# Kernel optimization log

Measured on AMD Instinct MI355X. Metric: run time of the kernel, lower is better.

The kernel has to match this reference:

```python
import jax, jax.numpy as jnp
import numpy as np

N_HEAD, D_MODEL, D_K, D_V = 16, 1024, 64, 64
LN_EPS = 1e-5


def setup_inputs() -> dict:
    key = jax.random.key(0)
    ks = jax.random.split(key, 7)
    B, L = 2, 2048
    q = jax.random.normal(ks[0], (B, L, N_HEAD * D_K), dtype=jnp.float32)
    k = jax.random.normal(ks[1], (B, L, N_HEAD * D_K), dtype=jnp.float32)
    v = jax.random.normal(ks[2], (B, L, N_HEAD * D_V), dtype=jnp.float32)
    # fc: Linear(d_v*n_head -> d_model)
    lim = 1.0 / np.sqrt(N_HEAD * D_V)
    W_fc = jax.random.uniform(ks[3], (N_HEAD * D_V, D_MODEL), minval=-lim, maxval=lim, dtype=jnp.float32)
    b_fc = jax.random.uniform(ks[4], (D_MODEL,), minval=-lim, maxval=lim, dtype=jnp.float32)
    ln_gamma = jnp.ones((D_MODEL,), dtype=jnp.float32)
    ln_beta = jnp.zeros((D_MODEL,), dtype=jnp.float32)
    return {"q": q, "k": k, "v": v, "W_fc": W_fc, "b_fc": b_fc,
            "ln_gamma": ln_gamma, "ln_beta": ln_beta}


def reference(q, k, v, W_fc, b_fc, ln_gamma, ln_beta):
    B, Lq, _ = q.shape
    Lk = k.shape[1]
    residual = q
    # split heads: [B, L, H*D] -> [B, H, L, D]
    qh = q.reshape(B, Lq, N_HEAD, D_K).transpose(0, 2, 1, 3)
    kh = k.reshape(B, Lk, N_HEAD, D_K).transpose(0, 2, 1, 3)
    vh = v.reshape(B, Lk, N_HEAD, D_V).transpose(0, 2, 1, 3)
    temperature = jnp.sqrt(jnp.asarray(D_K, dtype=q.dtype))
    # [B, H, Lq, Lk] attention scores (materialized, as in the original)
    scores = jnp.einsum('bhqd,bhkd->bhqk', qh, kh) / temperature
    attn = jax.nn.softmax(scores, axis=-1)
    # dropout is identity at eval time
    out = jnp.einsum('bhqk,bhkd->bhqd', attn, vh)
    out = out.transpose(0, 2, 1, 3).reshape(B, Lq, N_HEAD * D_V)
    out = out @ W_fc + b_fc
    out = out + residual
    # LayerNorm over d_model
    mu = jnp.mean(out, axis=-1, keepdims=True)
    var = jnp.var(out, axis=-1, keepdims=True)
    out = (out - mu) * jax.lax.rsqrt(var + LN_EPS) * ln_gamma + ln_beta
    return (out, attn)
```

## Files before the change

kernel.cpp:

```cpp
#include <hip/hip_runtime.h>
#include <hip/hip_bf16.h>
#include <math.h>

#define B_      2
#define L_      2048
#define H_      16
#define DMODEL_ 1024
#define LN_EPS  1e-5f

typedef __attribute__((ext_vector_type(8))) __bf16 bf16x8;
typedef __attribute__((ext_vector_type(8))) short  short8;
typedef __attribute__((ext_vector_type(4))) short  short4_t;
typedef __attribute__((ext_vector_type(4))) float  f32x4;

typedef const __attribute__((address_space(1))) void cgvoid_t;
typedef __attribute__((address_space(3))) void svoid_t;

__device__ __forceinline__ void gload16(const void* g, void* l) {
    __builtin_amdgcn_global_load_lds((cgvoid_t*)g, (svoid_t*)l, 16, 0, 0);
}
__device__ __forceinline__ short f2bf(float x) {
    __hip_bfloat16 h = __float2bfloat16(x);
    return __builtin_bit_cast(short, h);
}
__device__ __forceinline__ float bf2f(short s) {
    unsigned u = ((unsigned)(unsigned short)s) << 16;
    return __builtin_bit_cast(float, u);
}
__device__ __forceinline__ f32x4 mfma16(bf16x8 a, bf16x8 b, f32x4 c) {
    return __builtin_amdgcn_mfma_f32_16x16x32_bf16(a, b, c, 0, 0, 0);
}

__global__ __launch_bounds__(256) void prep_qk(const float* __restrict__ src,
                                               short* __restrict__ dst)
{
    const int t = blockIdx.x * 256 + threadIdx.x;
    const int c = t & 7, l = (t >> 3) & 2047, h = (t >> 14) & 15, b = t >> 18;
    const float* s = src + ((size_t)(b * L_ + l)) * DMODEL_ + h * 64 + c * 8;
    float4 f0 = *(const float4*)s;
    float4 f1 = *(const float4*)(s + 4);
    short8 o;
    o[0] = f2bf(f0.x); o[1] = f2bf(f0.y); o[2] = f2bf(f0.z); o[3] = f2bf(f0.w);
    o[4] = f2bf(f1.x); o[5] = f2bf(f1.y); o[6] = f2bf(f1.z); o[7] = f2bf(f1.w);
    short* d = dst + ((size_t)((b * H_ + h) * L_ + l)) * 64 + (c ^ (l & 7)) * 8;
    *(short8*)d = o;
}

__global__ __launch_bounds__(256) void prep_v(const float* __restrict__ src,
                                              short* __restrict__ dst)
{
    const int blk = blockIdx.x;
    const int g = blk & 63, h = (blk >> 6) & 15, b = blk >> 10;
    const int d = threadIdx.x & 63, lc = g * 4 + (threadIdx.x >> 6);
    const int l0 = lc * 8;
    const float* s = src + ((size_t)(b * L_ + l0)) * DMODEL_ + h * 64 + d;
    short8 o;
    #pragma unroll
    for (int j = 0; j < 8; ++j) o[j] = f2bf(s[(size_t)j * DMODEL_]);
    short* dp = dst + ((size_t)((b * H_ + h) * 64 + d)) * L_
              + (l0 & ~63) + (((lc & 7) ^ (d & 7)) * 8);
    *(short8*)dp = o;
}

__global__ __launch_bounds__(256) void prep_w(const float* __restrict__ W,
                                              short* __restrict__ Wh,
                                              short* __restrict__ Wl)
{
    const int t = blockIdx.x * 256 + threadIdx.x;
    const int n = t & 1023, kc = t >> 10;
    short8 oh, ol;
    #pragma unroll
    for (int e = 0; e < 8; ++e) {
        float wv = W[(size_t)(kc * 8 + e) * 1024 + n];
        short hs = f2bf(wv);
        oh[e] = hs;
        ol[e] = f2bf(wv - bf2f(hs));
    }
    const size_t off = (size_t)n * 1024 + (kc >> 3) * 64 + (((kc & 7) ^ (n & 7)) * 8);
    *(short8*)(Wh + off) = oh;
    *(short8*)(Wl + off) = ol;
}

__global__ __launch_bounds__(256) void attn_mfma(
    const short* __restrict__ Qb, const short* __restrict__ Kb,
    const short* __restrict__ Vb, float* __restrict__ attn,
    short* __restrict__ head)
{
    const int bid = blockIdx.x;
    const int g = (bid & 7) * 128 + (bid >> 3);
    const int qt = g & 31, bh = g >> 5;
    const int h = bh & 15, b = bh >> 4;

    const int tid = threadIdx.x;
    const int lane = tid & 63, w = tid >> 6;
    const int kgrp = lane >> 4, l15 = lane & 15;
    const int q0 = qt * 64;

    __shared__ short qe_s[64 * 64];
    __shared__ short k2_s[2 * 64 * 64];
    __shared__ short v2_s[2 * 64 * 64];

    const char* Qg = (const char*)(Qb + ((size_t)bh * L_ + q0) * 64);
    const char* Kg = (const char*)(Kb + (size_t)bh * L_ * 64);
    const char* Vg = (const char*)(Vb + (size_t)bh * 64 * L_);

    gload16(Qg + (w * 64 + lane) * 16, (char*)qe_s + w * 1024 + lane * 16);
    gload16(Qg + 4096 + (w * 64 + lane) * 16,
            (char*)qe_s + 4096 + w * 1024 + lane * 16);
    __syncthreads();

    const int prow = w * 16 + l15;
    bf16x8 bq0 = *(const bf16x8*)((const char*)qe_s + prow * 128 + ((kgrp ^ (prow & 7)) * 16));
    bf16x8 bq1 = *(const bf16x8*)((const char*)qe_s + prow * 128 + (((kgrp + 4) ^ (prow & 7)) * 16));
    __syncthreads();

    auto stageK = [&](int kt, int bu) {
        const char* kg = Kg + (size_t)kt * 8192;
        char* lk = (char*)k2_s + bu * 8192;
        gload16(kg + (w * 64 + lane) * 16, lk + w * 1024 + lane * 16);
        gload16(kg + 4096 + (w * 64 + lane) * 16, lk + 4096 + w * 1024 + lane * 16);
    };
    auto stageV = [&](int kt, int bu) {
        const char* vg = Vg + (size_t)kt * 128;
        char* lv = (char*)v2_s + bu * 8192;
        int cid = w * 64 + lane;
        gload16(vg + (size_t)(cid >> 3) * 4096 + (cid & 7) * 16, lv + w * 1024 + lane * 16);
        cid += 256;
        gload16(vg + (size_t)(cid >> 3) * 4096 + (cid & 7) * 16, lv + 4096 + w * 1024 + lane * 16);
    };

    float rsum = 0.f;
    stageK(0, 0);
    __syncthreads();
    int buf = 0;
    for (int kt = 0; kt < 32; ++kt) {
        if (kt < 31) stageK(kt + 1, buf ^ 1);
        const char* ks = (const char*)k2_s + buf * 8192;
        #pragma unroll
        for (int t = 0; t < 4; ++t) {
            const int brow = t * 16 + l15;
            f32x4 acc = {0.f, 0.f, 0.f, 0.f};
            bf16x8 k0 = *(const bf16x8*)(ks + brow * 128 + ((kgrp ^ (brow & 7)) * 16));
            bf16x8 k1 = *(const bf16x8*)(ks + brow * 128 + (((kgrp + 4) ^ (brow & 7)) * 16));
            acc = mfma16(k0, bq0, acc);
            acc = mfma16(k1, bq1, acc);
            #pragma unroll
            for (int r = 0; r < 4; ++r) rsum += __expf(acc[r] * 0.125f);
        }
        __syncthreads();
        buf ^= 1;
    }
    rsum += __shfl_xor(rsum, 16, 64);
    rsum += __shfl_xor(rsum, 32, 64);
    const float rinv = 1.0f / rsum;

    f32x4 oacc[4];
    #pragma unroll
    for (int t = 0; t < 4; ++t) oacc[t] = (f32x4){0.f, 0.f, 0.f, 0.f};

    float* arow_p = attn + ((size_t)bh * L_ + q0 + prow) * L_;
    char* pbase = (char*)qe_s + prow * 128;
    const int pswz0 = (kgrp ^ (prow & 7)) * 16;
    const int pswz1 = ((kgrp + 4) ^ (prow & 7)) * 16;

    stageK(0, 0);
    stageV(0, 0);
    __syncthreads();
    buf = 0;
    for (int kt = 0; kt < 32; ++kt) {
        if (kt < 31) { stageK(kt + 1, buf ^ 1); stageV(kt + 1, buf ^ 1); }
        const char* ks = (const char*)k2_s + buf * 8192;
        const char* vs = (const char*)v2_s + buf * 8192;
        #pragma unroll
        for (int t = 0; t < 4; ++t) {
            const int brow = t * 16 + l15;
            f32x4 acc = {0.f, 0.f, 0.f, 0.f};
            bf16x8 k0 = *(const bf16x8*)(ks + brow * 128 + ((kgrp ^ (brow & 7)) * 16));
            bf16x8 k1 = *(const bf16x8*)(ks + brow * 128 + (((kgrp + 4) ^ (brow & 7)) * 16));
            acc = mfma16(k0, bq0, acc);
            acc = mfma16(k1, bq1, acc);
            f32x4 ev;
            ev[0] = __expf(acc[0] * 0.125f) * rinv;
            ev[1] = __expf(acc[1] * 0.125f) * rinv;
            ev[2] = __expf(acc[2] * 0.125f) * rinv;
            ev[3] = __expf(acc[3] * 0.125f) * rinv;
            __builtin_nontemporal_store(ev,
                (f32x4*)(arow_p + kt * 64 + t * 16 + kgrp * 4));
            short4_t pk;
            pk[0] = f2bf(ev[0]); pk[1] = f2bf(ev[1]);
            pk[2] = f2bf(ev[2]); pk[3] = f2bf(ev[3]);
            const int pc = (t * 2 + (kgrp >> 1)) ^ (prow & 7);
            *(short4_t*)((char*)qe_s + prow * 128 + pc * 16 + (kgrp & 1) * 8) = pk;
        }
        bf16x8 pa0 = *(const bf16x8*)(pbase + pswz0);
        bf16x8 pa1 = *(const bf16x8*)(pbase + pswz1);
        #pragma unroll
        for (int t = 0; t < 4; ++t) {
            const int brow = t * 16 + l15;
            bf16x8 v0 = *(const bf16x8*)(vs + brow * 128 + ((kgrp ^ (brow & 7)) * 16));
            bf16x8 v1 = *(const bf16x8*)(vs + brow * 128 + (((kgrp + 4) ^ (brow & 7)) * 16));
            oacc[t] = mfma16(pa0, v0, oacc[t]);
            oacc[t] = mfma16(pa1, v1, oacc[t]);
        }
        __syncthreads();
        buf ^= 1;
    }

    #pragma unroll
    for (int t = 0; t < 4; ++t) {
        #pragma unroll
        for (int r = 0; r < 4; ++r) {
            const int rowidx = b * L_ + q0 + w * 16 + kgrp * 4 + r;
            const int dl = t * 16 + l15;
            head[(size_t)rowidx * 1024 + h * 64
                 + (((dl >> 3) ^ (rowidx & 7)) * 8) + (dl & 7)] = f2bf(oacc[t][r]);
        }
    }
}

__global__ __launch_bounds__(256) void fc_mfma(
    const short* __restrict__ Xs, const short* __restrict__ Wh,
    const short* __restrict__ Wl, const float* __restrict__ bias,
    const float* __restrict__ Qres, float* __restrict__ Y)
{
    const int n0 = blockIdx.x * 64, tok0 = blockIdx.y * 64;
    const int tid = threadIdx.x;
    const int lane = tid & 63, w = tid >> 6;
    const int kgrp = lane >> 4, l15 = lane & 15;

    __shared__ short x2_s[2 * 64 * 64];
    __shared__ short wh2_s[2 * 64 * 64];
    __shared__ short wl2_s[2 * 64 * 64];

    auto stageX = [&](int kt, int bu) {
        const char* xg = (const char*)Xs + (size_t)tok0 * 2048 + kt * 128;
        char* lx = (char*)x2_s + bu * 8192;
        int cid = w * 64 + lane;
        gload16(xg + (size_t)(cid >> 3) * 2048 + (cid & 7) * 16, lx + w * 1024 + lane * 16);
        cid += 256;
        gload16(xg + (size_t)(cid >> 3) * 2048 + (cid & 7) * 16, lx + 4096 + w * 1024 + lane * 16);
    };
    auto stageW = [&](int kt, int bu) {
        const char* wgh = (const char*)Wh + (size_t)n0 * 2048 + kt * 128;
        const char* wgl = (const char*)Wl + (size_t)n0 * 2048 + kt * 128;
        char* lh = (char*)wh2_s + bu * 8192;
        char* ll = (char*)wl2_s + bu * 8192;
        int cid = w * 64 + lane;
        const int ldst = w * 1024 + lane * 16;
        size_t go = (size_t)(cid >> 3) * 2048 + (cid & 7) * 16;
        gload16(wgh + go, lh + ldst);
        gload16(wgl + go, ll + ldst);
        cid += 256;
        go = (size_t)(cid >> 3) * 2048 + (cid & 7) * 16;
        gload16(wgh + go, lh + 4096 + ldst);
        gload16(wgl + go, ll + 4096 + ldst);
    };

    f32x4 oacc[4];
    #pragma unroll
    for (int t = 0; t < 4; ++t) oacc[t] = (f32x4){0.f, 0.f, 0.f, 0.f};

    stageX(0, 0);
    stageW(0, 0);
    __syncthreads();
    int buf = 0;
    const int xrow = w * 16 + l15;
    for (int kt = 0; kt < 16; ++kt) {
        if (kt < 15) { stageX(kt + 1, buf ^ 1); stageW(kt + 1, buf ^ 1); }
        const char* xs = (const char*)x2_s + buf * 8192;
        const char* wh = (const char*)wh2_s + buf * 8192;
        const char* wl = (const char*)wl2_s + buf * 8192;
        bf16x8 bx0 = *(const bf16x8*)(xs + xrow * 128 + ((kgrp ^ (xrow & 7)) * 16));
        bf16x8 bx1 = *(const bf16x8*)(xs + xrow * 128 + (((kgrp + 4) ^ (xrow & 7)) * 16));
        #pragma unroll
        for (int nt = 0; nt < 4; ++nt) {
            const int wrow = nt * 16 + l15;
            const int s0 = wrow * 128 + ((kgrp ^ (wrow & 7)) * 16);
            const int s1 = wrow * 128 + (((kgrp + 4) ^ (wrow & 7)) * 16);
            oacc[nt] = mfma16(*(const bf16x8*)(wh + s0), bx0, oacc[nt]);
            oacc[nt] = mfma16(*(const bf16x8*)(wh + s1), bx1, oacc[nt]);
            oacc[nt] = mfma16(*(const bf16x8*)(wl + s0), bx0, oacc[nt]);
            oacc[nt] = mfma16(*(const bf16x8*)(wl + s1), bx1, oacc[nt]);
        }
        __syncthreads();
        buf ^= 1;
    }

    const int tok = tok0 + w * 16 + l15;
    #pragma unroll
    for (int nt = 0; nt < 4; ++nt) {
        const int n = n0 + nt * 16 + kgrp * 4;
        float4 bb = *(const float4*)(bias + n);
        float4 qq = *(const float4*)(Qres + (size_t)tok * DMODEL_ + n);
        float4 yy;
        yy.x = oacc[nt][0] + bb.x + qq.x;
        yy.y = oacc[nt][1] + bb.y + qq.y;
        yy.z = oacc[nt][2] + bb.z + qq.z;
        yy.w = oacc[nt][3] + bb.w + qq.w;
        *(float4*)(Y + (size_t)tok * DMODEL_ + n) = yy;
    }
}

__global__ __launch_bounds__(256) void ln_kernel(
    const float* __restrict__ Y, const float* __restrict__ gamma,
    const float* __restrict__ beta, float* __restrict__ Out)
{
    const int tok = blockIdx.x * 4 + (threadIdx.x >> 6);
    const int lane = threadIdx.x & 63;
    const float4* yp = (const float4*)(Y + (size_t)tok * DMODEL_);
    float4 vv[4];
    float s = 0.f, s2 = 0.f;
    #pragma unroll
    for (int i = 0; i < 4; ++i) {
        vv[i] = yp[i * 64 + lane];
        s  += vv[i].x + vv[i].y + vv[i].z + vv[i].w;
        s2 += vv[i].x * vv[i].x + vv[i].y * vv[i].y
            + vv[i].z * vv[i].z + vv[i].w * vv[i].w;
    }
    #pragma unroll
    for (int m = 1; m < 64; m <<= 1) {
        s  += __shfl_xor(s,  m, 64);
        s2 += __shfl_xor(s2, m, 64);
    }
    const float mu   = s * (1.f / DMODEL_);
    const float var  = s2 * (1.f / DMODEL_) - mu * mu;
    const float rstd = rsqrtf(var + LN_EPS);
    const float4* g4 = (const float4*)gamma;
    const float4* b4 = (const float4*)beta;
    float4* op = (float4*)(Out + (size_t)tok * DMODEL_);
    #pragma unroll
    for (int i = 0; i < 4; ++i) {
        const int idx = i * 64 + lane;
        float4 g = g4[idx], be = b4[idx], o;
        o.x = (vv[i].x - mu) * rstd * g.x + be.x;
        o.y = (vv[i].y - mu) * rstd * g.y + be.y;
        o.z = (vv[i].z - mu) * rstd * g.z + be.z;
        o.w = (vv[i].w - mu) * rstd * g.w + be.w;
        op[idx] = o;
    }
}

extern "C" void kernel_launch(void* const* d_in, const int* in_sizes, int n_in,
                              void* d_out, int out_size, void* d_ws, size_t ws_size,
                              hipStream_t stream)
{
    const float* q     = (const float*)d_in[0];
    const float* k     = (const float*)d_in[1];
    const float* v     = (const float*)d_in[2];
    const float* W_fc  = (const float*)d_in[3];
    const float* b_fc  = (const float*)d_in[4];
    const float* gamma = (const float*)d_in[5];
    const float* beta  = (const float*)d_in[6];

    char* ws = (char*)d_ws;
    short* qb   = (short*)(ws);
    short* kb   = (short*)(ws + 8388608);
    short* vb   = (short*)(ws + 16777216);
    short* head = (short*)(ws + 25165824);
    short* whi  = (short*)(ws + 33554432);
    short* wlo  = (short*)(ws + 35651584);
    float* y    = (float*)(ws + 37748736);

    float* out  = (float*)d_out;
    float* attn = out + (size_t)B_ * L_ * DMODEL_;

    prep_qk<<<2048, 256, 0, stream>>>(q, qb);
    prep_qk<<<2048, 256, 0, stream>>>(k, kb);
    prep_v <<<2048, 256, 0, stream>>>(v, vb);
    prep_w <<<512,  256, 0, stream>>>(W_fc, whi, wlo);

    attn_mfma<<<1024, 256, 0, stream>>>(qb, kb, vb, attn, head);

    fc_mfma<<<dim3(16, 64), 256, 0, stream>>>(head, whi, wlo, b_fc, q, y);

    ln_kernel<<<1024, 256, 0, stream>>>(y, gamma, beta, out);
}
```

Measured before the change: 731.6 us.

## Double query tile per block, transpose V via shared memory, raise MFMA priority

The attention and FC kernels now run 512 threads (8 waves) per block and cover 128 query/token rows each, so every staged K/V or W tile is reused by twice as many rows and global staging traffic drops. prep_v now stages a 64x64 fp32 tile in padded shared memory and writes the transpose from there, replacing the old strided per-element global reads. s_setprio is raised around the MFMA loops so matrix work wins issue over other waves. The larger blocks use more LDS and registers, which may cut occupancy and halve the block count.

```diff
diff --git a/kernel.cpp b/kernel.cpp
--- a/kernel.cpp
+++ b/kernel.cpp
@@ -50,16 +50,37 @@
                                               short* __restrict__ dst)
 {
     const int blk = blockIdx.x;
-    const int g = blk & 63, h = (blk >> 6) & 15, b = blk >> 10;
-    const int d = threadIdx.x & 63, lc = g * 4 + (threadIdx.x >> 6);
-    const int l0 = lc * 8;
-    const float* s = src + ((size_t)(b * L_ + l0)) * DMODEL_ + h * 64 + d;
-    short8 o;
-    #pragma unroll
-    for (int j = 0; j < 8; ++j) o[j] = f2bf(s[(size_t)j * DMODEL_]);
-    short* dp = dst + ((size_t)((b * H_ + h) * 64 + d)) * L_
-              + (l0 & ~63) + (((lc & 7) ^ (d & 7)) * 8);
-    *(short8*)dp = o;
+    const int lt = blk & 31, h = (blk >> 5) & 15, b = blk >> 9;
+    const int l0 = lt * 64;
+    const int t = threadIdx.x;
+
+    __shared__ float tile[64][65];
+
+    {
+        const int row = t >> 2, seg = t & 3;
+        const float4* s = (const float4*)(src
+            + ((size_t)(b * L_ + l0 + row)) * DMODEL_ + h * 64 + seg * 16);
+        #pragma unroll
+        for (int i = 0; i < 4; ++i) {
+            float4 v = s[i];
+            tile[row][seg * 16 + i * 4 + 0] = v.x;
+            tile[row][seg * 16 + i * 4 + 1] = v.y;
+            tile[row][seg * 16 + i * 4 + 2] = v.z;
+            tile[row][seg * 16 + i * 4 + 3] = v.w;
+        }
+    }
+    __syncthreads();
+
+    const int d = t >> 2, p = t & 3;
+    short* drow = dst + ((size_t)((b * H_ + h) * 64 + d)) * L_ + l0;
+    #pragma unroll
+    for (int cc = 0; cc < 2; ++cc) {
+        const int c = p + cc * 4;
+        short8 o;
+        #pragma unroll
+        for (int j = 0; j < 8; ++j) o[j] = f2bf(tile[c * 8 + j][d]);
+        *(short8*)(drow + ((c ^ (d & 7)) * 8)) = o;
+    }
 }
 
 __global__ __launch_bounds__(256) void prep_w(const float* __restrict__ W,
@@ -81,22 +102,22 @@
     *(short8*)(Wl + off) = ol;
 }
 
-__global__ __launch_bounds__(256) void attn_mfma(
+__global__ __launch_bounds__(512) void attn_mfma(
     const short* __restrict__ Qb, const short* __restrict__ Kb,
     const short* __restrict__ Vb, float* __restrict__ attn,
     short* __restrict__ head)
 {
     const int bid = blockIdx.x;
-    const int g = (bid & 7) * 128 + (bid >> 3);
-    const int qt = g & 31, bh = g >> 5;
+    const int g = (bid & 7) * 64 + (bid >> 3);
+    const int qt = g & 15, bh = g >> 4;
     const int h = bh & 15, b = bh >> 4;
 
     const int tid = threadIdx.x;
     const int lane = tid & 63, w = tid >> 6;
     const int kgrp = lane >> 4, l15 = lane & 15;
-    const int q0 = qt * 64;
-
-    __shared__ short qe_s[64 * 64];
+    const int q0 = qt * 128;
+
+    __shared__ short qe_s[128 * 64];
     __shared__ short k2_s[2 * 64 * 64];
     __shared__ short v2_s[2 * 64 * 64];
 
@@ -104,9 +125,8 @@
     const char* Kg = (const char*)(Kb + (size_t)bh * L_ * 64);
     const char* Vg = (const char*)(Vb + (size_t)bh * 64 * L_);
 
-    gload16(Qg + (w * 64 + lane) * 16, (char*)qe_s + w * 1024 + lane * 16);
-    gload16(Qg + 4096 + (w * 64 + lane) * 16,
-            (char*)qe_s + 4096 + w * 1024 + lane * 16);
+    gload16(Qg + tid * 16, (char*)qe_s + tid * 16);
+    gload16(Qg + 8192 + tid * 16, (char*)qe_s + 8192 + tid * 16);
     __syncthreads();
 
     const int prow = w * 16 + l15;
@@ -115,18 +135,12 @@
     __syncthreads();
 
     auto stageK = [&](int kt, int bu) {
-        const char* kg = Kg + (size_t)kt * 8192;
-        char* lk = (char*)k2_s + bu * 8192;
-        gload16(kg + (w * 64 + lane) * 16, lk + w * 1024 + lane * 16);
-        gload16(kg + 4096 + (w * 64 + lane) * 16, lk + 4096 + w * 1024 + lane * 16);
+        gload16(Kg + (size_t)kt * 8192 + tid * 16,
+                (char*)k2_s + bu * 8192 + tid * 16);
     };
     auto stageV = [&](int kt, int bu) {
-        const char* vg = Vg + (size_t)kt * 128;
-        char* lv = (char*)v2_s + bu * 8192;
-        int cid = w * 64 + lane;
-        gload16(vg + (size_t)(cid >> 3) * 4096 + (cid & 7) * 16, lv + w * 1024 + lane * 16);
-        cid += 256;
-        gload16(vg + (size_t)(cid >> 3) * 4096 + (cid & 7) * 16, lv + 4096 + w * 1024 + lane * 16);
+        gload16(Vg + (size_t)kt * 128 + (size_t)(tid >> 3) * 4096 + (tid & 7) * 16,
+                (char*)v2_s + bu * 8192 + tid * 16);
     };
 
     float rsum = 0.f;
@@ -194,6 +208,7 @@
         }
         bf16x8 pa0 = *(const bf16x8*)(pbase + pswz0);
         bf16x8 pa1 = *(const bf16x8*)(pbase + pswz1);
+        __builtin_amdgcn_s_setprio(1);
         #pragma unroll
         for (int t = 0; t < 4; ++t) {
             const int brow = t * 16 + l15;
@@ -202,6 +217,7 @@
             oacc[t] = mfma16(pa0, v0, oacc[t]);
             oacc[t] = mfma16(pa1, v1, oacc[t]);
         }
+        __builtin_amdgcn_s_setprio(0);
         __syncthreads();
         buf ^= 1;
     }
@@ -218,42 +234,32 @@
     }
 }
 
-__global__ __launch_bounds__(256) void fc_mfma(
+__global__ __launch_bounds__(512) void fc_mfma(
     const short* __restrict__ Xs, const short* __restrict__ Wh,
     const short* __restrict__ Wl, const float* __restrict__ bias,
     const float* __restrict__ Qres, float* __restrict__ Y)
 {
-    const int n0 = blockIdx.x * 64, tok0 = blockIdx.y * 64;
+    const int n0 = blockIdx.x * 64, tok0 = blockIdx.y * 128;
     const int tid = threadIdx.x;
     const int lane = tid & 63, w = tid >> 6;
     const int kgrp = lane >> 4, l15 = lane & 15;
 
-    __shared__ short x2_s[2 * 64 * 64];
+    __shared__ short x2_s[2 * 128 * 64];
     __shared__ short wh2_s[2 * 64 * 64];
     __shared__ short wl2_s[2 * 64 * 64];
 
     auto stageX = [&](int kt, int bu) {
         const char* xg = (const char*)Xs + (size_t)tok0 * 2048 + kt * 128;
-        char* lx = (char*)x2_s + bu * 8192;
-        int cid = w * 64 + lane;
-        gload16(xg + (size_t)(cid >> 3) * 2048 + (cid & 7) * 16, lx + w * 1024 + lane * 16);
-        cid += 256;
-        gload16(xg + (size_t)(cid >> 3) * 2048 + (cid & 7) * 16, lx + 4096 + w * 1024 + lane * 16);
+        char* lx = (char*)x2_s + bu * 16384;
+        gload16(xg + (size_t)(tid >> 3) * 2048 + (tid & 7) * 16, lx + tid * 16);
+        const int cid = tid + 512;
+        gload16(xg + (size_t)(cid >> 3) * 2048 + (cid & 7) * 16, lx + 8192 + tid * 16);
     };
     auto stageW = [&](int kt, int bu) {
-        const char* wgh = (const char*)Wh + (size_t)n0 * 2048 + kt * 128;
-        const char* wgl = (const char*)Wl + (size_t)n0 * 2048 + kt * 128;
-        char* lh = (char*)wh2_s + bu * 8192;
-        char* ll = (char*)wl2_s + bu * 8192;
-        int cid = w * 64 + lane;
-        const int ldst = w * 1024 + lane * 16;
-        size_t go = (size_t)(cid >> 3) * 2048 + (cid & 7) * 16;
-        gload16(wgh + go, lh + ldst);
-        gload16(wgl + go, ll + ldst);
-        cid += 256;
-        go = (size_t)(cid >> 3) * 2048 + (cid & 7) * 16;
-        gload16(wgh + go, lh + 4096 + ldst);
-        gload16(wgl + go, ll + 4096 + ldst);
+        const size_t go = (size_t)n0 * 2048 + kt * 128
+                        + (size_t)(tid >> 3) * 2048 + (tid & 7) * 16;
+        gload16((const char*)Wh + go, (char*)wh2_s + bu * 8192 + tid * 16);
+        gload16((const char*)Wl + go, (char*)wl2_s + bu * 8192 + tid * 16);
     };
 
     f32x4 oacc[4];
@@ -267,11 +273,12 @@
     const int xrow = w * 16 + l15;
     for (int kt = 0; kt < 16; ++kt) {
         if (kt < 15) { stageX(kt + 1, buf ^ 1); stageW(kt + 1, buf ^ 1); }
-        const char* xs = (const char*)x2_s + buf * 8192;
+        const char* xs = (const char*)x2_s + buf * 16384;
         const char* wh = (const char*)wh2_s + buf * 8192;
         const char* wl = (const char*)wl2_s + buf * 8192;
         bf16x8 bx0 = *(const bf16x8*)(xs + xrow * 128 + ((kgrp ^ (xrow & 7)) * 16));
         bf16x8 bx1 = *(const bf16x8*)(xs + xrow * 128 + (((kgrp + 4) ^ (xrow & 7)) * 16));
+        __builtin_amdgcn_s_setprio(1);
         #pragma unroll
         for (int nt = 0; nt < 4; ++nt) {
             const int wrow = nt * 16 + l15;
@@ -282,6 +289,7 @@
             oacc[nt] = mfma16(*(const bf16x8*)(wl + s0), bx0, oacc[nt]);
             oacc[nt] = mfma16(*(const bf16x8*)(wl + s1), bx1, oacc[nt]);
         }
+        __builtin_amdgcn_s_setprio(0);
         __syncthreads();
         buf ^= 1;
     }
@@ -366,12 +374,12 @@
 
     prep_qk<<<2048, 256, 0, stream>>>(q, qb);
     prep_qk<<<2048, 256, 0, stream>>>(k, kb);
-    prep_v <<<2048, 256, 0, stream>>>(v, vb);
+    prep_v <<<1024, 256, 0, stream>>>(v, vb);
     prep_w <<<512,  256, 0, stream>>>(W_fc, whi, wlo);
 
-    attn_mfma<<<1024, 256, 0, stream>>>(qb, kb, vb, attn, head);
-
-    fc_mfma<<<dim3(16, 64), 256, 0, stream>>>(head, whi, wlo, b_fc, q, y);
+    attn_mfma<<<512, 512, 0, stream>>>(qb, kb, vb, attn, head);
+
+    fc_mfma<<<dim3(16, 32), 512, 0, stream>>>(head, whi, wlo, b_fc, q, y);
 
     ln_kernel<<<1024, 256, 0, stream>>>(y, gamma, beta, out);
 }
```

Result: no change. 725.0 us (-0.9%).
